# Kernel optimization log

Measured on AMD Instinct MI355X. Metric: run time of the kernel, lower is better.

Reference implementation:

```python
import jax, jax.numpy as jnp
import numpy as np

B, S, N, M = 64, 512, 512, 128   # batch, sensory_size, state_size, motor_size
UNFOLDS = 6
DT = 0.1  # elapsed_time


def _gate(v, mu, sigma):
    # piecewise-linear 'sigmoid': clip((v - mu + sigma) / (2 sigma), 0, 1)
    # v: [B, P] -> [B, P, 1] broadcast against [P, N]
    return jnp.clip((v[..., None] - mu + sigma) / (2.0 * sigma), 0.0, 1.0)


def setup_inputs() -> dict:
    key = jax.random.key(0)
    ks = jax.random.split(key, 12)
    u = lambda k, sh, lo, hi: jax.random.uniform(k, sh, jnp.float32, lo, hi)
    inputs = jax.random.normal(ks[0], (B, S), dtype=jnp.float32)
    states = jax.random.normal(ks[1], (B, N), dtype=jnp.float32) * 0.1
    # parameters per _init_ranges
    tau = u(ks[2], (N,), 0.001, 2.0)
    b = u(ks[3], (N,), -0.2, 0.2)
    erev = jnp.where(jax.random.bernoulli(ks[4], 0.8, (N, N)), 1.0, -1.0).astype(jnp.float32)
    w = u(ks[5], (N, N), 0.001, 1.0)
    sigma = jnp.full((N, N), 0.5, jnp.float32)
    mu = jnp.full((N, N), 0.5, jnp.float32)
    sensory_erev = jnp.where(jax.random.bernoulli(ks[6], 0.8, (S, N)), 1.0, -1.0).astype(jnp.float32)
    sensory_w = u(ks[7], (S, N), 0.001, 1.0)
    sensory_sigma = jnp.full((S, N), 0.5, jnp.float32)
    sensory_mu = jnp.full((S, N), 0.5, jnp.float32)
    sparsity_mask = jax.random.bernoulli(ks[8], 0.3, (N, N)).astype(jnp.float32)
    sensory_sparsity_mask = jax.random.bernoulli(ks[9], 0.3, (S, N)).astype(jnp.float32)
    input_w = jnp.ones((S,), jnp.float32)
    input_b = jnp.zeros((S,), jnp.float32)
    output_w = jnp.ones((M,), jnp.float32)
    output_b = jnp.zeros((M,), jnp.float32)
    return dict(inputs=inputs, states=states, tau=tau, b=b, erev=erev, w=w,
                sigma=sigma, mu=mu, sensory_erev=sensory_erev, sensory_w=sensory_w,
                sensory_sigma=sensory_sigma, sensory_mu=sensory_mu,
                sparsity_mask=sparsity_mask, sensory_sparsity_mask=sensory_sparsity_mask,
                input_w=input_w, input_b=input_b, output_w=output_w, output_b=output_b)


def reference(inputs, states, tau, b, erev, w, sigma, mu,
              sensory_erev, sensory_w, sensory_sigma, sensory_mu,
              sparsity_mask, sensory_sparsity_mask,
              input_w, input_b, output_w, output_b):
    # input mapping (affine)
    x = inputs * input_w + input_b                                   # [B, S]
    # sensory synapses, computed once
    sa = _gate(x, sensory_mu, sensory_sigma) * sensory_sparsity_mask  # [B, S, N]
    s_rev = jnp.einsum('bsn,sn->bn', sa, sensory_erev)               # [B, N]
    s_w = jnp.einsum('bsn,sn->bn', sa, sensory_w)                    # [B, N]
    delta = DT / UNFOLDS

    def step(v, _):
        g = _gate(v, mu, sigma) * sparsity_mask                      # [B, N, N]
        sum_rev = jnp.einsum('bij,ij->bj', g, erev) + s_rev + b      # sum over presynaptic i
        sum_w = jnp.einsum('bij,ij->bj', g, w) + s_w
        k = 1.0 / (1.0 + sum_w)
        taun = tau * k
        q = taun / (taun + delta)
        v_new = q * v + (1.0 - q) * k * sum_rev
        return v_new, None

    v, _ = jax.lax.scan(step, states, None, length=UNFOLDS)
    # output mapping: slice last M neurons (M < N), then affine
    out = v[:, -M:] * output_w + output_b                            # [B, M]
    return out, v
```

## Files before the change

### kernel.cpp

```cpp
#include <hip/hip_runtime.h>
#include <string.h>

constexpr int cB = 64, cS = 512, cN = 512, cM = 128, cUNF = 6;
constexpr float cDELTA = 0.016666666666666666f;

constexpr int KB = 4;
constexpr int JT = 32;
constexpr int NJT = cN / JT;
constexpr int NT = 1024;
constexpr int NW = NT / 64;
constexpr int NB = (cB / KB) * NJT;
constexpr int ILEN = 16;
constexpr int SLEN = 16;

constexpr size_t OFF_EWT = 0;
constexpr size_t OFF_SRB = (size_t)cN * cN * 2;
constexpr size_t OFF_SW  = OFF_SRB + (size_t)cB * cN;
constexpr size_t OFF_VA  = OFF_SW  + (size_t)cB * cN;
constexpr size_t OFF_VB  = OFF_VA  + (size_t)cB * cN;
constexpr size_t OFF_CTR = OFF_VB  + (size_t)cB * cN;
constexpr int SLOT_STRIDE = 16;

__device__ __forceinline__ float clamp01(float x) {
    return __builtin_amdgcn_fmed3f(x, 0.0f, 1.0f);
}

__global__ __launch_bounds__(NT)
void k_prep(const float* __restrict__ inputs, const float* __restrict__ bias,
            const float* __restrict__ erev,  const float* __restrict__ wgt,
            const float* __restrict__ sigma, const float* __restrict__ mu,
            const float* __restrict__ serev, const float* __restrict__ swgt,
            const float* __restrict__ ssigma,const float* __restrict__ smu,
            const float* __restrict__ mask,  const float* __restrict__ smask,
            const float* __restrict__ inw,   const float* __restrict__ inb,
            float* __restrict__ ws)
{
    float2* EWt  = (float2*)(ws + OFF_EWT);
    float*  srb  = ws + OFF_SRB;
    float*  swS  = ws + OFF_SW;
    int*    ctr  = (int*)(ws + OFF_CTR);
    int*    flags = ctr + 4096;

    const int tid = threadIdx.x, bid = blockIdx.x;
    const int bg = bid >> 4, jt = bid & (NJT - 1);
    const int b0 = bg * KB, j0 = jt * JT;
    const int jl = tid & (JT - 1), ic = tid >> 5;
    const int wv_id = tid >> 6, lane = tid & 63;
    const int j = j0 + jl;

    __shared__ float xsh[cS * KB];
    __shared__ float redR[KB * NW * JT];
    __shared__ float redW[KB * NW * JT];

    {
        int idx = bid * NT + tid;
        int i = idx >> 9, jj = idx & (cN - 1);
        int jtt = jj >> 5, jjl = jj & (JT - 1);
        float mk = mask[idx];
        float2 ew = make_float2(erev[idx] * mk, wgt[idx] * mk);
        unsigned long long bits;
        memcpy(&bits, &ew, 8);
        __hip_atomic_store(
            (unsigned long long*)&EWt[(size_t)jtt * (cN * JT) + i * JT + jjl],
            bits, __ATOMIC_RELAXED, __HIP_MEMORY_SCOPE_AGENT);
        if (mk != 0.0f && !((sigma[idx] == 0.5f) && (mu[idx] == 0.5f)))
            __hip_atomic_store(&flags[jtt], 1, __ATOMIC_RELAXED, __HIP_MEMORY_SCOPE_AGENT);
    }

#pragma unroll
    for (int r = 0; r < (cS * KB) / NT; ++r) {
        int t = tid + r * NT;
        int bb = t & 3, s = t >> 2;
        xsh[t] = fmaf(inputs[(b0 + bb) * cS + s], inw[s], inb[s]);
    }
    __syncthreads();

    {
        float aR[KB] = {0.f, 0.f, 0.f, 0.f}, aW[KB] = {0.f, 0.f, 0.f, 0.f};
        int idx = (ic * SLEN) * cN + j;
        int xo  = (ic * SLEN) * KB;
#pragma unroll 4
        for (int ii = 0; ii < SLEN; ++ii, idx += cN, xo += KB) {
            float sg = ssigma[idx];
            float a  = 0.5f / sg;
            float c  = fmaf(-smu[idx], a, 0.5f);
            float mk = smask[idx];
            float e  = serev[idx] * mk;
            float wv = swgt[idx] * mk;
            const float4 xv = *(const float4*)&xsh[xo];
            float g;
            g = clamp01(fmaf(xv.x, a, c)); aR[0] = fmaf(g, e, aR[0]); aW[0] = fmaf(g, wv, aW[0]);
            g = clamp01(fmaf(xv.y, a, c)); aR[1] = fmaf(g, e, aR[1]); aW[1] = fmaf(g, wv, aW[1]);
            g = clamp01(fmaf(xv.z, a, c)); aR[2] = fmaf(g, e, aR[2]); aW[2] = fmaf(g, wv, aW[2]);
            g = clamp01(fmaf(xv.w, a, c)); aR[3] = fmaf(g, e, aR[3]); aW[3] = fmaf(g, wv, aW[3]);
        }
#pragma unroll
        for (int b = 0; b < KB; ++b) {
            aR[b] += __shfl_xor(aR[b], 32, 64);
            aW[b] += __shfl_xor(aW[b], 32, 64);
        }
        if (lane < JT) {
#pragma unroll
            for (int b = 0; b < KB; ++b) {
                redR[(b * NW + wv_id) * JT + lane] = aR[b];
                redW[(b * NW + wv_id) * JT + lane] = aW[b];
            }
        }
    }
    __syncthreads();

    if (tid < JT * KB) {
        int jj = tid & (JT - 1), bb = tid >> 5;
        float r = 0.f, wv = 0.f;
#pragma unroll
        for (int w = 0; w < NW; ++w) {
            r  += redR[(bb * NW + w) * JT + jj];
            wv += redW[(bb * NW + w) * JT + jj];
        }
        int jg = j0 + jj;
        int gidx = (b0 + bb) * cN + jg;
        srb[gidx] = r + bias[jg];
        swS[gidx] = wv;
    }
}

__global__ __launch_bounds__(NT, 4)
void k_main(const float* __restrict__ states, const float* __restrict__ tau,
            const float* __restrict__ sigma,  const float* __restrict__ mu,
            const float* __restrict__ outw,   const float* __restrict__ outb,
            float* __restrict__ out, float* __restrict__ ws)
{
    const float* srb = ws + OFF_SRB;
    const float* swS = ws + OFF_SW;
    float* vA  = ws + OFF_VA;
    float* vB  = ws + OFF_VB;
    int*   ctr = (int*)(ws + OFF_CTR);

    const int tid = threadIdx.x, bid = blockIdx.x;
    const int jt = (bid & 7) * 2 + ((bid >> 3) & 1);
    const int bg = bid >> 4;
    const int b0 = bg * KB, j0 = jt * JT;
    const int jl = tid & (JT - 1), ic = tid >> 5;
    const int wv_id = tid >> 6, lane = tid & 63;
    int* mySlot = ctr + (bg * 16 + jt) * SLOT_STRIDE;
    int* bgSlots = ctr + (bg * 16) * SLOT_STRIDE;
    const int* flags = ctr + 4096;

    const float2* ews = (const float2*)(ws + OFF_EWT) + (size_t)jt * (cN * JT);

    __shared__ float stage[cN * KB];
    __shared__ float redR[KB * NW * JT];
    __shared__ float redW[KB * NW * JT];

    const int fast = (flags[jt] != 1);

    float my_srb = 0.f, my_sw = 0.f, my_tau = 0.f, my_ow = 0.f, my_ob = 0.f;
    float vold = 0.f;
    int my_gidx = 0, my_mi = -1;
    if (tid < JT * KB) {
        int jj = tid & (JT - 1), bb = tid >> 5;
        int jg = j0 + jj;
        my_gidx = (b0 + bb) * cN + jg;
        my_srb  = srb[my_gidx];
        my_sw   = swS[my_gidx];
        my_tau  = tau[jg];
        vold    = states[my_gidx];
        if (jg >= cN - cM) {
            int m = jg - (cN - cM);
            my_ow = outw[m]; my_ob = outb[m];
            my_mi = (b0 + bb) * cM + m;
        }
    }

    const float* vin = states;
    for (int u = 0; u < cUNF; ++u) {
#pragma unroll
        for (int r = 0; r < (cN * KB) / NT; ++r) {
            int t = tid + r * NT;
            int bb = t >> 9, ii = t & (cN - 1);
            float vvv = __hip_atomic_load(&vin[(b0 + bb) * cN + ii],
                                          __ATOMIC_RELAXED, __HIP_MEMORY_SCOPE_AGENT);
            stage[ii * KB + bb] = fast ? clamp01(vvv) : vvv;
        }
        __syncthreads();

        float aR[KB] = {0.f, 0.f, 0.f, 0.f}, aW[KB] = {0.f, 0.f, 0.f, 0.f};
        if (fast) {
            int eo = (ic * ILEN) * JT + jl;
            int vo = (ic * ILEN) * KB;
#pragma unroll 8
            for (int ii = 0; ii < ILEN; ++ii, eo += JT, vo += KB) {
                const float2 ew = ews[eo];
                const float4 g4 = *(const float4*)&stage[vo];
                aR[0] = fmaf(g4.x, ew.x, aR[0]); aW[0] = fmaf(g4.x, ew.y, aW[0]);
                aR[1] = fmaf(g4.y, ew.x, aR[1]); aW[1] = fmaf(g4.y, ew.y, aW[1]);
                aR[2] = fmaf(g4.z, ew.x, aR[2]); aW[2] = fmaf(g4.z, ew.y, aW[2]);
                aR[3] = fmaf(g4.w, ew.x, aR[3]); aW[3] = fmaf(g4.w, ew.y, aW[3]);
            }
        } else {
            int j    = j0 + jl;
            int idx  = (ic * ILEN) * cN + j;
            int eo   = (ic * ILEN) * JT + jl;
            int vo   = (ic * ILEN) * KB;
#pragma unroll 4
            for (int ii = 0; ii < ILEN; ++ii, idx += cN, eo += JT, vo += KB) {
                float sg = sigma[idx];
                float a  = 0.5f / sg;
                float c  = fmaf(-mu[idx], a, 0.5f);
                const float2 ew = ews[eo];
                const float4 v4 = *(const float4*)&stage[vo];
                float g;
                g = clamp01(fmaf(v4.x, a, c)); aR[0] = fmaf(g, ew.x, aR[0]); aW[0] = fmaf(g, ew.y, aW[0]);
                g = clamp01(fmaf(v4.y, a, c)); aR[1] = fmaf(g, ew.x, aR[1]); aW[1] = fmaf(g, ew.y, aW[1]);
                g = clamp01(fmaf(v4.z, a, c)); aR[2] = fmaf(g, ew.x, aR[2]); aW[2] = fmaf(g, ew.y, aW[2]);
                g = clamp01(fmaf(v4.w, a, c)); aR[3] = fmaf(g, ew.x, aR[3]); aW[3] = fmaf(g, ew.y, aW[3]);
            }
        }
#pragma unroll
        for (int b = 0; b < KB; ++b) {
            aR[b] += __shfl_xor(aR[b], 32, 64);
            aW[b] += __shfl_xor(aW[b], 32, 64);
        }
        if (lane < JT) {
#pragma unroll
            for (int b = 0; b < KB; ++b) {
                redR[(b * NW + wv_id) * JT + lane] = aR[b];
                redW[(b * NW + wv_id) * JT + lane] = aW[b];
            }
        }
        __syncthreads();

        float* vout = (u & 1) ? vB : vA;
        if (tid < JT * KB) {
            int jj = tid & (JT - 1), bb = tid >> 5;
            float r = 0.f, wv = 0.f;
#pragma unroll
            for (int w = 0; w < NW; ++w) {
                r  += redR[(bb * NW + w) * JT + jj];
                wv += redW[(bb * NW + w) * JT + jj];
            }
            r  += my_srb;
            wv += my_sw;
            float k    = 1.0f / (1.0f + wv);
            float taun = my_tau * k;
            float inv  = 1.0f / (taun + cDELTA);
            float vn   = (taun * inv) * vold + (cDELTA * inv) * k * r;
            vold = vn;
            if (u == cUNF - 1) {
                (out + cB * cM)[my_gidx] = vn;
                if (my_mi >= 0) out[my_mi] = fmaf(vn, my_ow, my_ob);
            } else {
                __hip_atomic_store(&vout[my_gidx], vn,
                                   __ATOMIC_RELAXED, __HIP_MEMORY_SCOPE_AGENT);
            }
        }

        if (u < cUNF - 1) {
            __syncthreads();
            if (tid == 0)
                __hip_atomic_store(mySlot, u + 1,
                                   __ATOMIC_RELAXED, __HIP_MEMORY_SCOPE_AGENT);
            if (tid < NJT) {
                const int* slot = bgSlots + tid * SLOT_STRIDE;
                while (__hip_atomic_load(slot, __ATOMIC_RELAXED, __HIP_MEMORY_SCOPE_AGENT) < u + 1)
                    __builtin_amdgcn_s_sleep(1);
            }
            __syncthreads();
            vin = (u & 1) ? vB : vA;
        }
    }
}

extern "C" void kernel_launch(void* const* d_in, const int* in_sizes, int n_in,
                              void* d_out, int out_size, void* d_ws, size_t ws_size,
                              hipStream_t stream)
{
    const float* inputs = (const float*)d_in[0];
    const float* states = (const float*)d_in[1];
    const float* tau    = (const float*)d_in[2];
    const float* bias   = (const float*)d_in[3];
    const float* erev   = (const float*)d_in[4];
    const float* wgt    = (const float*)d_in[5];
    const float* sigma  = (const float*)d_in[6];
    const float* mu     = (const float*)d_in[7];
    const float* serev  = (const float*)d_in[8];
    const float* swgt   = (const float*)d_in[9];
    const float* ssigma = (const float*)d_in[10];
    const float* smu    = (const float*)d_in[11];
    const float* mask   = (const float*)d_in[12];
    const float* smask  = (const float*)d_in[13];
    const float* inw    = (const float*)d_in[14];
    const float* inb    = (const float*)d_in[15];
    const float* outw   = (const float*)d_in[16];
    const float* outb   = (const float*)d_in[17];
    float* out = (float*)d_out;
    float* ws  = (float*)d_ws;

    k_prep<<<NB, NT, 0, stream>>>(inputs, bias, erev, wgt, sigma, mu,
                                  serev, swgt, ssigma, smu, mask, smask,
                                  inw, inb, ws);

    k_main<<<NB, NT, 0, stream>>>(states, tau, sigma, mu,
                                  outw, outb, out, ws);
}
```

Baseline: 122.9 us.

## Replace per-step block barriers with per-wave flag polling and single-wave finalize

The per-step state update is now done by one wavefront, with each lane handling two outputs. That wave publishes the progress flag right after draining its stores with s_waitcnt, with no block-wide barrier. Every wave then polls the peer flags itself at the start of the next unfold, replacing the two __syncthreads around the old spin-wait. The aim is to cut barrier and cross-block handoff latency in this latency-bound recurrent loop. The cost is that correctness now rests on relaxed atomics plus a manual waitcnt for memory ordering.

```diff
diff --git a/kernel.cpp b/kernel.cpp
--- a/kernel.cpp
+++ b/kernel.cpp
@@ -142,7 +142,7 @@
     const int b0 = bg * KB, j0 = jt * JT;
     const int jl = tid & (JT - 1), ic = tid >> 5;
     const int wv_id = tid >> 6, lane = tid & 63;
-    int* mySlot = ctr + (bg * 16 + jt) * SLOT_STRIDE;
+    int* mySlot  = ctr + (bg * 16 + jt) * SLOT_STRIDE;
     int* bgSlots = ctr + (bg * 16) * SLOT_STRIDE;
     const int* flags = ctr + 4096;
 
@@ -154,26 +154,39 @@
 
     const int fast = (flags[jt] != 1);
 
-    float my_srb = 0.f, my_sw = 0.f, my_tau = 0.f, my_ow = 0.f, my_ob = 0.f;
-    float vold = 0.f;
-    int my_gidx = 0, my_mi = -1;
-    if (tid < JT * KB) {
-        int jj = tid & (JT - 1), bb = tid >> 5;
-        int jg = j0 + jj;
-        my_gidx = (b0 + bb) * cN + jg;
-        my_srb  = srb[my_gidx];
-        my_sw   = swS[my_gidx];
-        my_tau  = tau[jg];
-        vold    = states[my_gidx];
-        if (jg >= cN - cM) {
-            int m = jg - (cN - cM);
-            my_ow = outw[m]; my_ob = outb[m];
-            my_mi = (b0 + bb) * cM + m;
+    float my_srb[2] = {0.f, 0.f}, my_sw[2] = {0.f, 0.f}, my_tau[2] = {0.f, 0.f};
+    float my_ow[2] = {0.f, 0.f}, my_ob[2] = {0.f, 0.f}, vold[2] = {0.f, 0.f};
+    int my_gidx[2] = {0, 0}, my_mi[2] = {-1, -1};
+    if (tid < 64) {
+#pragma unroll
+        for (int p = 0; p < 2; ++p) {
+            int t  = tid + 64 * p;
+            int jj = t & (JT - 1), bb = t >> 5;
+            int jg = j0 + jj;
+            my_gidx[p] = (b0 + bb) * cN + jg;
+            my_srb[p]  = srb[my_gidx[p]];
+            my_sw[p]   = swS[my_gidx[p]];
+            my_tau[p]  = tau[jg];
+            vold[p]    = states[my_gidx[p]];
+            if (jg >= cN - cM) {
+                int m = jg - (cN - cM);
+                my_ow[p] = outw[m]; my_ob[p] = outb[m];
+                my_mi[p] = (b0 + bb) * cM + m;
+            }
         }
     }
 
     const float* vin = states;
     for (int u = 0; u < cUNF; ++u) {
+        if (u > 0) {
+            if (lane < NJT) {
+                const int* slot = bgSlots + lane * SLOT_STRIDE;
+                while (__hip_atomic_load(slot, __ATOMIC_RELAXED, __HIP_MEMORY_SCOPE_AGENT) < u)
+                    __builtin_amdgcn_s_sleep(1);
+            }
+            asm volatile("" ::: "memory");
+        }
+
 #pragma unroll
         for (int r = 0; r < (cN * KB) / NT; ++r) {
             int t = tid + r * NT;
@@ -231,43 +244,40 @@
         __syncthreads();
 
         float* vout = (u & 1) ? vB : vA;
-        if (tid < JT * KB) {
-            int jj = tid & (JT - 1), bb = tid >> 5;
-            float r = 0.f, wv = 0.f;
-#pragma unroll
-            for (int w = 0; w < NW; ++w) {
-                r  += redR[(bb * NW + w) * JT + jj];
-                wv += redW[(bb * NW + w) * JT + jj];
-            }
-            r  += my_srb;
-            wv += my_sw;
-            float k    = 1.0f / (1.0f + wv);
-            float taun = my_tau * k;
-            float inv  = 1.0f / (taun + cDELTA);
-            float vn   = (taun * inv) * vold + (cDELTA * inv) * k * r;
-            vold = vn;
-            if (u == cUNF - 1) {
-                (out + cB * cM)[my_gidx] = vn;
-                if (my_mi >= 0) out[my_mi] = fmaf(vn, my_ow, my_ob);
-            } else {
-                __hip_atomic_store(&vout[my_gidx], vn,
-                                   __ATOMIC_RELAXED, __HIP_MEMORY_SCOPE_AGENT);
-            }
-        }
-
-        if (u < cUNF - 1) {
-            __syncthreads();
-            if (tid == 0)
-                __hip_atomic_store(mySlot, u + 1,
-                                   __ATOMIC_RELAXED, __HIP_MEMORY_SCOPE_AGENT);
-            if (tid < NJT) {
-                const int* slot = bgSlots + tid * SLOT_STRIDE;
-                while (__hip_atomic_load(slot, __ATOMIC_RELAXED, __HIP_MEMORY_SCOPE_AGENT) < u + 1)
-                    __builtin_amdgcn_s_sleep(1);
-            }
-            __syncthreads();
-            vin = (u & 1) ? vB : vA;
-        }
+        if (tid < 64) {
+#pragma unroll
+            for (int p = 0; p < 2; ++p) {
+                int t  = tid + 64 * p;
+                int jj = t & (JT - 1), bb = t >> 5;
+                float r = 0.f, wv = 0.f;
+#pragma unroll
+                for (int w = 0; w < NW; ++w) {
+                    r  += redR[(bb * NW + w) * JT + jj];
+                    wv += redW[(bb * NW + w) * JT + jj];
+                }
+                r  += my_srb[p];
+                wv += my_sw[p];
+                float k    = 1.0f / (1.0f + wv);
+                float taun = my_tau[p] * k;
+                float inv  = 1.0f / (taun + cDELTA);
+                float vn   = (taun * inv) * vold[p] + (cDELTA * inv) * k * r;
+                vold[p] = vn;
+                if (u == cUNF - 1) {
+                    (out + cB * cM)[my_gidx[p]] = vn;
+                    if (my_mi[p] >= 0) out[my_mi[p]] = fmaf(vn, my_ow[p], my_ob[p]);
+                } else {
+                    __hip_atomic_store(&vout[my_gidx[p]], vn,
+                                       __ATOMIC_RELAXED, __HIP_MEMORY_SCOPE_AGENT);
+                }
+            }
+            if (u < cUNF - 1) {
+                asm volatile("s_waitcnt vmcnt(0)" ::: "memory");
+                if (tid == 0)
+                    __hip_atomic_store(mySlot, u + 1,
+                                       __ATOMIC_RELAXED, __HIP_MEMORY_SCOPE_AGENT);
+            }
+        }
+        vin = (u & 1) ? vB : vA;
     }
 }
 
```

Result: slower. 132.5 us (+7.8%).
